# Kernel tuning notes

Measured on AMD Instinct MI355X. Metric: run time of the kernel, lower is better.

Reference implementation:

```python
import jax, jax.numpy as jnp
import numpy as np

SR = 16000
FRAME = 400      # int(0.025*SR)
HOP = 160        # int(0.01*SR)
MINP, MAXP = 32, 320   # SR/500, SR/50
NFFT_FRAME = 1024      # next pow2 >= 2*FRAME-1
NFFT_FULL = 262144     # >= samples + max hnr lag (160000+200)
LN_EPS = 1e-5


def _frame(a):
    n = a.shape[0]
    nf = (n - FRAME - 1) // HOP + 1  # len(range(0, n-FRAME, HOP))
    idx = jnp.arange(nf)[:, None] * HOP + jnp.arange(FRAME)[None, :]
    return a[idx]  # [nf, FRAME]


def _autocorr(x, nfft, nlags):
    # linear autocorrelation via FFT; nfft >= len + nlags avoids circular wrap
    X = jnp.fft.rfft(x, n=nfft)
    ac = jnp.fft.irfft(X * jnp.conj(X), n=nfft)
    return ac[..., :nlags]


def _masked_mean_std(x, m):
    cnt = m.sum()
    c = jnp.maximum(cnt, 1.0)
    mean = jnp.sum(x * m) / c
    var = jnp.sum(((x - mean) ** 2) * m) / c
    return jnp.where(cnt > 0, mean, 0.0), jnp.where(cnt > 0, jnp.sqrt(var), 0.0)


def _compact(vals, mask, fill_len):
    # pack masked values to the front (stable); first k=sum(mask) entries valid
    rank = jnp.cumsum(mask) - 1
    idx = jnp.where(mask, rank, fill_len)
    return jnp.zeros(fill_len, vals.dtype).at[idx].set(vals, mode='drop')


def _prosody_single(a):
    n = a.shape[0]
    frames = _frame(a)
    nf = frames.shape[0]
    # --- energy ---
    rms = jnp.sqrt(jnp.mean(frames ** 2, axis=-1))
    e_mean, e_std = rms.mean(), rms.std()
    # --- zero-crossing rate ---
    zcr = jnp.sum(jnp.abs(jnp.diff(jnp.sign(frames), axis=-1)), axis=-1) / (2.0 * FRAME)
    z_mean, z_std = zcr.mean(), zcr.std()
    # --- F0 via per-frame autocorrelation peak picking ---
    ac = _autocorr(frames, NFFT_FRAME, MAXP)            # [nf, 320]
    peak = jnp.argmax(ac[:, MINP:MAXP], axis=-1) + MINP  # first max, like np.argmax
    ac_pk = jnp.take_along_axis(ac, peak[:, None], axis=-1)[:, 0]
    f0 = SR / peak.astype(jnp.float32)
    valid = (ac_pk > 0.3 * ac[:, 0]) & (f0 > 50.0) & (f0 < 500.0)
    f0_mean, f0_std = _masked_mean_std(f0, valid.astype(jnp.float32))
    # --- jitter: rising threshold crossings over the whole waveform ---
    thr = 0.3 * jnp.max(jnp.abs(a))
    cross = (a[:-1] < thr) & (a[1:] >= thr)  # crossing at index i in [1, n)
    pos = jnp.arange(1, n)
    k = cross.sum()
    posarr = _compact(pos, cross, n)
    periods = (posarr[1:] - posarr[:-1]).astype(jnp.float32)
    nper = k - 1
    pmask = jnp.arange(n - 1) < nper
    mean_period = jnp.sum(periods * pmask) / jnp.maximum(nper, 1)
    pdiffs = jnp.abs(periods[1:] - periods[:-1])
    dmask = jnp.arange(n - 2) < (nper - 1)
    mean_pdiff = jnp.sum(pdiffs * dmask) / jnp.maximum(nper - 1, 1)
    jitter = jnp.where((nper >= 2) & (mean_period > 0),
                       jnp.clip(mean_pdiff / jnp.maximum(mean_period, 1e-12), 0.0, 1.0), 0.0)
    jitter = jnp.where((f0_mean < 50.0) | (f0_mean > 500.0), 0.0, jitter)
    # --- shimmer: diffs of consecutive retained (>0.01) frame peak amps ---
    amp = jnp.max(jnp.abs(frames), axis=-1)
    amask = amp > 0.01
    ka = amask.sum()
    amparr = _compact(amp, amask, nf)
    adiffs = jnp.abs(amparr[1:] - amparr[:-1])
    admask = jnp.arange(nf - 1) < (ka - 1)
    mean_amp = jnp.sum(amparr * (jnp.arange(nf) < ka)) / jnp.maximum(ka, 1)
    mean_adiff = jnp.sum(adiffs * admask) / jnp.maximum(ka - 1, 1)
    shimmer = jnp.where((ka >= 2) & (mean_amp > 0),
                        jnp.clip(mean_adiff / jnp.maximum(mean_amp, 1e-12), 0.0, 1.0), 0.0)
    # --- HNR: full-signal autocorrelation, lags 50..199 ---
    seg = _autocorr(a, NFFT_FULL, 200)[50:200]
    sig_peak = jnp.max(seg)
    noise_floor = jnp.percentile(seg, 10.0)  # numpy-default linear interpolation
    hnr = jnp.where(noise_floor > 0,
                    jnp.clip(sig_peak / jnp.maximum(noise_floor, 1e-30) / 100.0, 0.0, 1.0), 0.0)
    # --- voicing rate (energy + zcr thresholds; source truncated, see notes) ---
    voiced = (rms > 0.01) & (zcr < 0.3)
    voicing_rate = voiced.mean()
    feats = jnp.stack([f0_mean / 500.0, f0_std / 100.0, e_mean, e_std,
                       z_mean, z_std, jitter, shimmer, hnr, voicing_rate])
    metrics = jnp.stack([f0_mean, f0_std, e_mean, e_std, z_mean, z_std,
                         jitter, shimmer, hnr, voicing_rate])
    return feats, metrics


def _project(feats, W1, b1, gamma, beta, W2, b2):
    h = feats @ W1.T + b1
    mu = h.mean(-1, keepdims=True)
    var = h.var(-1, keepdims=True)
    h = (h - mu) / jnp.sqrt(var + LN_EPS) * gamma + beta
    h = jax.nn.relu(h)          # dropout = identity (eval mode)
    return h @ W2.T + b2


def setup_inputs() -> dict:
    key = jax.random.key(0)
    ks = jax.random.split(key, 7)
    B, N = 128, 160000
    return {
        'raw_audio': jax.random.normal(ks[0], (B, N), dtype=jnp.float32) * 0.5,
        'W1': jax.random.normal(ks[1], (64, 10), dtype=jnp.float32) * 0.3,
        'b1': jax.random.normal(ks[2], (64,), dtype=jnp.float32) * 0.01,
        'gamma': jnp.ones((64,), dtype=jnp.float32),
        'beta': jnp.zeros((64,), dtype=jnp.float32),
        'W2': jax.random.normal(ks[3], (128, 64), dtype=jnp.float32) * 0.1,
        'b2': jax.random.normal(ks[4], (128,), dtype=jnp.float32) * 0.01,
    }


def reference(raw_audio, W1, b1, gamma, beta, W2, b2):
    feats, metrics = jax.vmap(_prosody_single)(raw_audio)  # [B,10], [B,10]
    feats = jax.lax.stop_gradient(feats)  # torch detaches via numpy round-trip
    proj = _project(feats, W1, b1, gamma, beta, W2, b2)    # [B,128]
    return proj, metrics
```

## Files before the change

kernel.cpp:

```cpp
#include <hip/hip_runtime.h>
#include <stdint.h>

typedef unsigned int uint;
typedef unsigned short ushort;
typedef unsigned long long ull;
typedef __attribute__((ext_vector_type(8))) short bf16x8;
typedef __attribute__((ext_vector_type(4))) float f32x4;

#define SR_F 16000.0f
#define NSAMP 160000
#define NB 128
#define FRAME 400
#define HOP 160
#define NF 998
#define NHNR_CHUNK 10
#define JCH 125
#define HNR_LAGS 150
#define TJ 25
#define HWIN (32*TJ + 304)
#define NJB 10
#define TAIL0 ((NF - 1) * HOP + FRAME)

#define HXO 562
#define HREG 1116

#define OFF_RMS 0
#define OFF_ZCR (OFF_RMS + NB*NF)
#define OFF_AMP (OFF_ZCR + NB*NF)
#define OFF_F0  (OFF_AMP + NB*NF)
#define OFF_VAL (OFF_F0  + NB*NF)
#define OFF_HNR (OFF_VAL + NB*NF)
#define OFF_JST (OFF_HNR + NB*NHNR_CHUNK*HNR_LAGS)

__device__ __forceinline__ int imax_(int a, int b) { return a > b ? a : b; }
__device__ __forceinline__ int imin2_(int a, int b) { return a < b ? a : b; }

__device__ __forceinline__ int   f2i(float v) { return __builtin_bit_cast(int, v); }
__device__ __forceinline__ float i2f(int v)   { return __builtin_bit_cast(float, v); }
__device__ __forceinline__ uint  f2u(float v) { return __builtin_bit_cast(uint, v); }

#if __has_builtin(__builtin_amdgcn_permlane16_swap) && __has_builtin(__builtin_amdgcn_permlane32_swap)
#define HAVE_PLSWAP 1
#endif

template<int C>
__device__ __forceinline__ int dpp_i(int x) {
    return __builtin_amdgcn_update_dpp(0, x, C, 0xf, 0xf, true);
}
template<int C>
__device__ __forceinline__ float dpp_f(float x) { return i2f(dpp_i<C>(f2i(x))); }

__device__ __forceinline__ float wred_sum(float x) {
#ifdef HAVE_PLSWAP
    x += dpp_f<0xB1>(x);
    x += dpp_f<0x4E>(x);
    x += dpp_f<0x141>(x);
    x += dpp_f<0x140>(x);
    {
        auto r = __builtin_amdgcn_permlane16_swap(f2i(x), f2i(x), false, false);
        x = i2f((int)r[0]) + i2f((int)r[1]);
    }
    {
        auto r = __builtin_amdgcn_permlane32_swap(f2i(x), f2i(x), false, false);
        x = i2f((int)r[0]) + i2f((int)r[1]);
    }
#else
    #pragma unroll
    for (int off = 32; off; off >>= 1) x += __shfl_xor(x, off);
#endif
    return x;
}

__device__ __forceinline__ float wred_max(float x) {
#ifdef HAVE_PLSWAP
    x = fmaxf(x, dpp_f<0xB1>(x));
    x = fmaxf(x, dpp_f<0x4E>(x));
    x = fmaxf(x, dpp_f<0x141>(x));
    x = fmaxf(x, dpp_f<0x140>(x));
    {
        auto r = __builtin_amdgcn_permlane16_swap(f2i(x), f2i(x), false, false);
        x = fmaxf(i2f((int)r[0]), i2f((int)r[1]));
    }
    {
        auto r = __builtin_amdgcn_permlane32_swap(f2i(x), f2i(x), false, false);
        x = fmaxf(i2f((int)r[0]), i2f((int)r[1]));
    }
#else
    #pragma unroll
    for (int off = 32; off; off >>= 1) x = fmaxf(x, __shfl_xor(x, off));
#endif
    return x;
}

__device__ __forceinline__ int wred_imin(int x) {
#ifdef HAVE_PLSWAP
    x = imin2_(x, dpp_i<0xB1>(x));
    x = imin2_(x, dpp_i<0x4E>(x));
    x = imin2_(x, dpp_i<0x141>(x));
    x = imin2_(x, dpp_i<0x140>(x));
    {
        auto r = __builtin_amdgcn_permlane16_swap(x, x, false, false);
        x = imin2_((int)r[0], (int)r[1]);
    }
    {
        auto r = __builtin_amdgcn_permlane32_swap(x, x, false, false);
        x = imin2_((int)r[0], (int)r[1]);
    }
#else
    #pragma unroll
    for (int off = 32; off; off >>= 1) x = imin2_(x, __shfl_xor(x, off));
#endif
    return x;
}

__device__ __forceinline__ uint cvtpk_bf16(float a, float b) {
    uint r;
    asm("v_cvt_pk_bf16_f32 %0, %1, %2" : "=v"(r) : "v"(a), "v"(b));
    return r;
}

__device__ __forceinline__ bf16x8 ld_b_frag(const uint* p) {
    union { uint u[4]; bf16x8 v; } t;
    t.u[0] = p[0]; t.u[1] = p[1]; t.u[2] = p[2]; t.u[3] = p[3];
    return t.v;
}

__device__ __forceinline__ int sx_(float a, float b) {
    return (int)((f2u(a) ^ f2u(b)) >> 31);
}

struct JSt { int cnt, p0, p1, pl, pl2; float sum; };

__device__ __forceinline__ void jmerge(JSt& A, const JSt& r) {
    if (r.cnt == 0) return;
    if (A.cnt == 0) { A = r; return; }
    int pb = r.p0 - A.pl;
    A.sum += r.sum;
    if (A.cnt >= 2) A.sum += fabsf((float)(pb - (A.pl - A.pl2)));
    if (r.cnt >= 2) A.sum += fabsf((float)((r.p1 - r.p0) - pb));
    if (A.cnt == 1) A.p1 = r.p0;
    A.pl2 = (r.cnt >= 2) ? r.pl2 : A.pl;
    A.pl = r.pl;
    A.cnt += r.cnt;
}

__device__ __forceinline__ JSt jword(unsigned long long word, int wb) {
    JSt st; st.cnt = 0; st.p0 = 0; st.p1 = 0; st.pl = 0; st.pl2 = 0; st.sum = 0.f;
    while (word) {
        int b = __builtin_ctzll(word);
        word &= word - 1;
        int pos = wb + b + 1;
        if (st.cnt >= 2) st.sum += fabsf((float)((pos - st.pl) - (st.pl - st.pl2)));
        if (st.cnt == 0) st.p0 = pos;
        if (st.cnt == 1) st.p1 = pos;
        st.pl2 = st.pl; st.pl = pos; ++st.cnt;
    }
    return st;
}

__global__ __launch_bounds__(256) void k_frame(const float* __restrict__ audio,
                                               float* __restrict__ ws, int xoff)
{
    __shared__ __align__(16) uint lds[4][744];
    const int tid = threadIdx.x;
    const int widx = tid >> 6, lane = tid & 63;
    const int lo = lane & 15, q = lane >> 4;
    const int s = blockIdx.y;
    const int fbase = (blockIdx.x + xoff) * 16 + widx * 4;
    const float* as = audio + (size_t)s * NSAMP;

    uint* base = lds[widx];
    ull* zb = (ull*)base;
    const ushort* xw_us = (const ushort*)base;

    for (int i = lane; i < 168; i += 64) {
        int zi;
        if (i < 60)       zi = i;
        else if (i < 84)  zi = 160 + (i - 60);
        else if (i < 144) zi = 185 + (i - 84);
        else              zi = 345 + (i - 144);
        zb[zi] = 0ull;
    }

    float4 tA, tB; float bnA, bnB;
    {
        int f0 = fbase; if (f0 > NF - 1) f0 = NF - 1;
        const float* a = as + (size_t)f0 * HOP;
        tA  = ((const float4*)a)[lane];
        bnA = a[4 * lane + 4];
        tB.x = tB.y = tB.z = tB.w = 0.f; bnB = 0.f;
        if (lane < 36) {
            tB  = ((const float4*)a)[64 + lane];
            bnB = (lane < 35) ? a[4 * (64 + lane) + 4] : 0.f;
        }
    }

    for (int p = 0; p < 4; ++p) {
        int f = fbase + p; if (f > NF - 1) f = NF - 1;

        float amp; int zci;
        {
            amp = fmaxf(fmaxf(fabsf(tA.x), fabsf(tA.y)),
                        fmaxf(fabsf(tA.z), fabsf(tA.w)));
            zci = sx_(tA.x, tA.y) + sx_(tA.y, tA.z)
                + sx_(tA.z, tA.w) + sx_(tA.w, bnA);
            ull w = (ull)cvtpk_bf16(tA.x, tA.y) | ((ull)cvtpk_bf16(tA.z, tA.w) << 32);
            ull o = (ull)cvtpk_bf16(tA.y, tA.z) | ((ull)cvtpk_bf16(tA.w, bnA) << 32);
            zb[60 + lane]  = w;
            zb[245 + lane] = o;
        }
        if (lane < 36) {
            amp = fmaxf(amp, fmaxf(fmaxf(fabsf(tB.x), fabsf(tB.y)),
                                   fmaxf(fabsf(tB.z), fabsf(tB.w))));
            zci += sx_(tB.x, tB.y) + sx_(tB.y, tB.z) + sx_(tB.z, tB.w);
            if (lane < 35) zci += sx_(tB.w, bnB);
            ull w = (ull)cvtpk_bf16(tB.x, tB.y) | ((ull)cvtpk_bf16(tB.z, tB.w) << 32);
            ull o = (ull)cvtpk_bf16(tB.y, tB.z) | ((ull)cvtpk_bf16(tB.w, bnB) << 32);
            zb[124 + lane] = w;
            zb[309 + lane] = o;
        }
        float zcs = wred_sum((float)zci);
        amp = wred_max(amp);

        __syncthreads();

        float4 nA, nB; float nbA = 0.f, nbB = 0.f;
        nA.x = nA.y = nA.z = nA.w = 0.f; nB = nA;
        if (p < 3) {
            int fn = fbase + p + 1; if (fn > NF - 1) fn = NF - 1;
            const float* an = as + (size_t)fn * HOP;
            nA  = ((const float4*)an)[lane];
            nbA = an[4 * lane + 4];
            if (lane < 36) {
                nB  = ((const float4*)an)[64 + lane];
                nbB = (lane < 35) ? an[4 * (64 + lane) + 4] : 0.f;
            }
        }

        f32x4 acc1 = {0.f, 0.f, 0.f, 0.f};
        f32x4 acc2 = {0.f, 0.f, 0.f, 0.f};
        const int a_eb = 240 + 8 * q - 16 * lo;
        const uint* bp = base + ((lo & 1) ? 370 : 0) + 120 + 4 * q + (lo >> 1);
        bf16x8 ah[5];

        #pragma unroll
        for (int j = 0; j < 13; ++j) {
            bf16x8 a1 = *(const bf16x8*)(xw_us + a_eb + 32 * j);
            bf16x8 b  = ld_b_frag(bp + 16 * j);
            acc1 = __builtin_amdgcn_mfma_f32_16x16x32_bf16(a1, b, acc1, 0, 0, 0);
            if (j < 5) ah[j] = a1;
            if (j >= 8)
                acc2 = __builtin_amdgcn_mfma_f32_16x16x32_bf16(ah[j - 8], b, acc2, 0, 0, 0);
        }

        float ac0 = i2f(__builtin_amdgcn_readfirstlane(f2i(acc1[0])));

        float bv = -1e30f; int bl = 1 << 30;
        #pragma unroll
        for (int r = 0; r < 4; ++r) {
            int lag = 64 * q + 16 * r + lo;
            float v = acc1[r];
            bool ok = (r >= 2) || (q >= 1);
            if (ok && v > bv) { bv = v; bl = lag; }
        }
        if (q == 0) {
            #pragma unroll
            for (int r = 0; r < 4; ++r) {
                int lag = 256 + 16 * r + lo;
                float v = acc2[r];
                if (v > bv) { bv = v; bl = lag; }
            }
        }
        float mv = wred_max(bv);
        int   ml = wred_imin((bv == mv) ? bl : (1 << 30));

        if (lane == 0) {
            float f0v = SR_F / (float)ml;
            int valid = (mv > 0.3f * ac0) && (f0v > 50.f) && (f0v < 500.f);
            size_t idx = (size_t)s * NF + f;
            ws[OFF_RMS + idx] = sqrtf(fmaxf(ac0, 0.f) / (float)FRAME);
            ws[OFF_ZCR + idx] = zcs / 400.f;
            ws[OFF_AMP + idx] = amp;
            ws[OFF_F0  + idx] = f0v;
            ws[OFF_VAL + idx] = valid ? 1.f : 0.f;
        }

        tA = nA; tB = nB; bnA = nbA; bnB = nbB;
        __syncthreads();
    }
}

__global__ __launch_bounds__(256) void k_hnr(const float* __restrict__ audio,
                                             float* __restrict__ ws)
{
    __shared__ __align__(16) uint hxd[4][HREG];
    __shared__ unsigned long long msk[250];
    __shared__ __align__(16) uint pool[1504];
    __shared__ JSt sg[25];
    __shared__ float swmax[4];
    const int tid = threadIdx.x;
    const int widx = tid >> 6, lane = tid & 63;
    const int lo = lane & 15, q = lane >> 4;
    const int s = blockIdx.y;
    const int c = blockIdx.x * 4 + widx;
    const float* a = audio + (size_t)s * NSAMP;

    float (*hred)[152] = (float (*)[152])pool;
    JSt* sw = (JSt*)pool;

    uint* xwd = hxd[widx];
    uint* xod = hxd[widx] + HXO;
    const ushort* xw = (const ushort*)xwd;

    const int aoff = 240 + 8 * q - 16 * lo;
    const uint* bw = (lo & 1) ? xod : xwd;
    const int boff = 144 + 4 * q + (lo >> 1);

    f32x4 acc = {0.f, 0.f, 0.f, 0.f};

    for (int tile = 0; tile < JCH / TJ; ++tile) {
        const int g0 = 32 * (c * JCH + tile * TJ) - 288;
        for (int v = lane; v < HWIN / 4; v += 64) {
            int g = g0 + 4 * v;
            float x0, x1, x2, x3, x4;
            if (g >= 0 && g + 4 < NSAMP) {
                float4 t = *(const float4*)(a + g);
                x0 = t.x; x1 = t.y; x2 = t.z; x3 = t.w;
                x4 = a[g + 4];
            } else {
                x0 = (g     >= 0 && g     < NSAMP) ? a[g]     : 0.f;
                x1 = (g + 1 >= 0 && g + 1 < NSAMP) ? a[g + 1] : 0.f;
                x2 = (g + 2 >= 0 && g + 2 < NSAMP) ? a[g + 2] : 0.f;
                x3 = (g + 3 >= 0 && g + 3 < NSAMP) ? a[g + 3] : 0.f;
                x4 = (g + 4 >= 0 && g + 4 < NSAMP) ? a[g + 4] : 0.f;
            }
            int d = 2 * v;
            xwd[d] = cvtpk_bf16(x0, x1); xwd[d + 1] = cvtpk_bf16(x2, x3);
            xod[d] = cvtpk_bf16(x1, x2); xod[d + 1] = cvtpk_bf16(x3, x4);
        }
        asm volatile("" ::: "memory");
        __builtin_amdgcn_sched_barrier(0);

        #pragma unroll
        for (int jl = 0; jl < TJ; ++jl) {
            bf16x8 af = *(const bf16x8*)(xw + aoff + 32 * jl);
            bf16x8 bf = ld_b_frag(bw + boff + 16 * jl);
            acc = __builtin_amdgcn_mfma_f32_16x16x32_bf16(af, bf, acc, 0, 0, 0);
        }
        asm volatile("" ::: "memory");
        __builtin_amdgcn_sched_barrier(0);
    }

    #pragma unroll
    for (int r = 0; r < 4; ++r) {
        int row = 4 * q + r;
        int lag = 48 + 16 * row + lo;
        if (row < 10 && lag >= 50 && lag < 200)
            hred[widx][lag - 50] = acc[r];
    }
    __syncthreads();
    if (tid < HNR_LAGS) {
        float v = hred[0][tid] + hred[1][tid] + hred[2][tid] + hred[3][tid];
        ws[OFF_HNR + ((size_t)s * NHNR_CHUNK + blockIdx.x) * HNR_LAGS + tid] = v;
    }

    float m = 0.f;
    const float* ampA = ws + OFF_AMP + (size_t)s * NF;
    for (int i = tid; i < NF; i += 256) m = fmaxf(m, ampA[i]);
    if (tid < NSAMP - TAIL0) m = fmaxf(m, fabsf(a[TAIL0 + tid]));
    m = wred_max(m);
    if ((tid & 63) == 0) swmax[tid >> 6] = m;
    __syncthreads();
    const float thr = 0.3f * fmaxf(fmaxf(swmax[0], swmax[1]),
                                   fmaxf(swmax[2], swmax[3]));

    const int cbase = blockIdx.x * 16000;
    for (int ot = 0; ot < 9; ++ot) {
        float va[7], vb[7];
        #pragma unroll
        for (int k = 0; k < 7; ++k) {
            int off = (ot * 7 + k) * 256 + tid;
            int i = cbase + off;
            bool in = (off < 16000) && (i < NSAMP - 1);
            va[k] = in ? a[i] : 1e30f;
            vb[k] = in ? a[i + 1] : 1e30f;
        }
        #pragma unroll
        for (int k = 0; k < 7; ++k) {
            int off = (ot * 7 + k) * 256 + tid;
            bool fl = (va[k] < thr) && (vb[k] >= thr);
            unsigned long long bal = __ballot(fl);
            int w = off >> 6;
            if ((tid & 63) == 0 && w < 250) msk[w] = bal;
        }
    }
    __syncthreads();

    if (tid < 250) sw[tid] = jword(msk[tid], cbase + tid * 64);
    __syncthreads();
    if (tid < 25) {
        JSt A = sw[10 * tid];
        #pragma unroll
        for (int k = 1; k < 10; ++k) jmerge(A, sw[10 * tid + k]);
        sg[tid] = A;
    }
    __syncthreads();
    if (tid == 0) {
        JSt A = sg[0];
        for (int k = 1; k < 25; ++k) jmerge(A, sg[k]);
        float* jp = ws + OFF_JST + ((size_t)s * NJB + blockIdx.x) * 6;
        jp[0] = (float)A.cnt; jp[1] = (float)A.p0; jp[2] = (float)A.p1;
        jp[3] = (float)A.pl;  jp[4] = (float)A.pl2; jp[5] = A.sum;
    }
}

__global__ __launch_bounds__(256) void k_final(const float* __restrict__ ws,
        const float* __restrict__ W1, const float* __restrict__ b1,
        const float* __restrict__ gam, const float* __restrict__ bet,
        const float* __restrict__ W2, const float* __restrict__ b2,
        float* __restrict__ out)
{
    __shared__ float samp[NF];
    __shared__ float sac[HNR_LAGS];
    __shared__ float sred[32];
    __shared__ float sstat[11];
    __shared__ float sjit[4];
    __shared__ float sjst[NJB * 6];
    __shared__ float sfeats[10];
    __shared__ float shid[64];
    __shared__ float ssa[250][5];
    __shared__ float ssg[25][5];

    const int s = blockIdx.x;
    const int tid = threadIdx.x;
    const float* rmsA = ws + OFF_RMS + (size_t)s * NF;
    const float* zcrA = ws + OFF_ZCR + (size_t)s * NF;
    const float* ampA = ws + OFF_AMP + (size_t)s * NF;
    const float* f0A  = ws + OFF_F0  + (size_t)s * NF;
    const float* valA = ws + OFF_VAL + (size_t)s * NF;

    float a0=0,a1=0,a2=0,a3=0,a4=0,a5=0,a6=0,a7=0;
    for (int i = tid; i < NF; i += 256) {
        float r = rmsA[i], z = zcrA[i], f0 = f0A[i], v = valA[i];
        samp[i] = ampA[i];
        a0 += r; a1 += r * r; a2 += z; a3 += z * z;
        a4 += f0 * v; a5 += f0 * f0 * v; a6 += v;
        a7 += (r > 0.01f && z < 0.3f) ? 1.f : 0.f;
    }
    if (tid < NJB * 6) sjst[tid] = ws[OFF_JST + (size_t)s * NJB * 6 + tid];
    #pragma unroll
    for (int off = 32; off; off >>= 1) {
        a0 += __shfl_xor(a0, off); a1 += __shfl_xor(a1, off);
        a2 += __shfl_xor(a2, off); a3 += __shfl_xor(a3, off);
        a4 += __shfl_xor(a4, off); a5 += __shfl_xor(a5, off);
        a6 += __shfl_xor(a6, off); a7 += __shfl_xor(a7, off);
    }
    if ((tid & 63) == 0) {
        int w = tid >> 6;
        sred[w*8+0]=a0; sred[w*8+1]=a1; sred[w*8+2]=a2; sred[w*8+3]=a3;
        sred[w*8+4]=a4; sred[w*8+5]=a5; sred[w*8+6]=a6; sred[w*8+7]=a7;
    }
    __syncthreads();

    if (tid < HNR_LAGS) {
        float acc = 0.f;
        const float* p = ws + OFF_HNR + (size_t)s * NHNR_CHUNK * HNR_LAGS + tid;
        #pragma unroll
        for (int c = 0; c < NHNR_CHUNK; ++c) acc += p[c * HNR_LAGS];
        sac[tid] = acc;
    }
    if (tid == 0) {
        for (int k = 0; k < 8; ++k)
            sstat[k] = sred[k] + sred[8+k] + sred[16+k] + sred[24+k];
    }
    if (tid < 250) {
        int i0 = tid * 4;
        float cnt=0.f, first=0.f, last=0.f, ssum=0.f, sad=0.f;
        #pragma unroll
        for (int k = 0; k < 4; ++k) {
            int i = i0 + k;
            if (i < NF) {
                float av = samp[i];
                if (av > 0.01f) {
                    if (cnt >= 1.f) sad += fabsf(av - last);
                    else first = av;
                    ssum += av; last = av; cnt += 1.f;
                }
            }
        }
        ssa[tid][0]=cnt; ssa[tid][1]=first; ssa[tid][2]=last;
        ssa[tid][3]=ssum; ssa[tid][4]=sad;
    }
    __syncthreads();

    if (tid < HNR_LAGS) {
        float v = sac[tid];
        int r = 0;
        for (int j = 0; j < HNR_LAGS; ++j) {
            float vj = sac[j];
            r += (vj < v) || (vj == v && j < tid);
        }
        if (r == 14) sstat[8] = v;
        if (r == 15) sstat[9] = v;
    }
    if (tid == 160) {
        JSt A; A.cnt = 0; A.p0 = 0; A.p1 = 0; A.pl = 0; A.pl2 = 0; A.sum = 0.f;
        for (int c = 0; c < NJB; ++c) {
            JSt r;
            r.cnt = (int)sjst[c*6+0]; r.p0 = (int)sjst[c*6+1];
            r.p1  = (int)sjst[c*6+2]; r.pl = (int)sjst[c*6+3];
            r.pl2 = (int)sjst[c*6+4]; r.sum = sjst[c*6+5];
            jmerge(A, r);
        }
        sjit[0] = (float)A.cnt; sjit[1] = (float)A.p0;
        sjit[2] = (float)A.pl;  sjit[3] = A.sum;
    }
    if (tid == 192) {
        float mx = sac[0];
        for (int j = 1; j < HNR_LAGS; ++j) mx = fmaxf(mx, sac[j]);
        sstat[10] = mx;
    }
    if (tid >= 200 && tid < 225) {
        int t2 = tid - 200;
        float cnt=0.f, first=0.f, last=0.f, ssum=0.f, sad=0.f;
        #pragma unroll
        for (int k = 0; k < 10; ++k) {
            int j = 10 * t2 + k;
            float c2 = ssa[j][0];
            if (c2 > 0.f) {
                if (cnt > 0.f) sad += ssa[j][4] + fabsf(ssa[j][1] - last);
                else { first = ssa[j][1]; sad += ssa[j][4]; }
                ssum += ssa[j][3]; last = ssa[j][2]; cnt += c2;
            }
        }
        ssg[t2][0]=cnt; ssg[t2][1]=first; ssg[t2][2]=last;
        ssg[t2][3]=ssum; ssg[t2][4]=sad;
    }
    __syncthreads();

    if (tid == 0) {
        float S_r = sstat[0], S_r2 = sstat[1], S_z = sstat[2], S_z2 = sstat[3];
        float S_f = sstat[4], S_f2 = sstat[5], S_v = sstat[6], S_voi = sstat[7];
        float e_mean = S_r / (float)NF;
        float e_std  = sqrtf(fmaxf(S_r2 / (float)NF - e_mean * e_mean, 0.f));
        float z_mean = S_z / (float)NF;
        float z_std  = sqrtf(fmaxf(S_z2 / (float)NF - z_mean * z_mean, 0.f));
        float f0_mean = 0.f, f0_std = 0.f;
        if (S_v > 0.f) {
            f0_mean = S_f / S_v;
            f0_std  = sqrtf(fmaxf(S_f2 / S_v - f0_mean * f0_mean, 0.f));
        }
        int k = (int)sjit[0];
        float pp0 = sjit[1], ppl = sjit[2], psum = sjit[3];
        int nper = k - 1;
        float mean_period = (k >= 2) ? (ppl - pp0) / (float)(k - 1) : 0.f;
        float mean_pd = psum / (float)imax_(nper - 1, 1);
        float jit = (nper >= 2 && mean_period > 0.f)
            ? fminf(fmaxf(mean_pd / fmaxf(mean_period, 1e-12f), 0.f), 1.f) : 0.f;
        if (f0_mean < 50.f || f0_mean > 500.f) jit = 0.f;
        float noise = 0.1f * sstat[8] + 0.9f * sstat[9];
        float hnr = (noise > 0.f)
            ? fminf(fmaxf(sstat[10] / fmaxf(noise, 1e-30f) / 100.f, 0.f), 1.f) : 0.f;

        float cnt=0.f, first=0.f, last=0.f, ssum=0.f, sad=0.f;
        for (int c = 0; c < 25; ++c) {
            float c2 = ssg[c][0];
            if (c2 > 0.f) {
                if (cnt > 0.f) sad += ssg[c][4] + fabsf(ssg[c][1] - last);
                else { first = ssg[c][1]; sad += ssg[c][4]; }
                ssum += ssg[c][3]; last = ssg[c][2]; cnt += c2;
            }
        }
        int ka = (int)cnt;
        float mean_amp = ssum / (float)imax_(ka, 1);
        float mean_ad  = sad  / (float)imax_(ka - 1, 1);
        float shim = (ka >= 2 && mean_amp > 0.f)
            ? fminf(fmaxf(mean_ad / fmaxf(mean_amp, 1e-12f), 0.f), 1.f) : 0.f;
        float voice = S_voi / (float)NF;

        float mt[10] = {f0_mean, f0_std, e_mean, e_std, z_mean, z_std, jit, shim, hnr, voice};
        for (int i = 0; i < 10; ++i) out[NB * 128 + s * 10 + i] = mt[i];
        sfeats[0] = f0_mean / 500.f;
        sfeats[1] = f0_std / 100.f;
        for (int i = 2; i < 10; ++i) sfeats[i] = mt[i];
    }
    __syncthreads();

    if (tid < 64) {
        float h = b1[tid];
        #pragma unroll
        for (int i = 0; i < 10; ++i) h = fmaf(sfeats[i], W1[tid * 10 + i], h);
        float sum = h, sq = h * h;
        #pragma unroll
        for (int off = 32; off; off >>= 1) {
            sum += __shfl_xor(sum, off);
            sq  += __shfl_xor(sq, off);
        }
        float mu = sum / 64.f;
        float var = sq / 64.f - mu * mu;
        float hn = (h - mu) * rsqrtf(var + 1e-5f) * gam[tid] + bet[tid];
        shid[tid] = fmaxf(hn, 0.f);
    }
    __syncthreads();
    if (tid < 128) {
        float accv = b2[tid];
        #pragma unroll 8
        for (int j = 0; j < 64; ++j) accv = fmaf(shid[j], W2[tid * 64 + j], accv);
        out[(size_t)s * 128 + tid] = accv;
    }
}

extern "C" void kernel_launch(void* const* d_in, const int* in_sizes, int n_in,
                              void* d_out, int out_size, void* d_ws, size_t ws_size,
                              hipStream_t stream)
{
    const float* audio = (const float*)d_in[0];
    const float* W1    = (const float*)d_in[1];
    const float* b1    = (const float*)d_in[2];
    const float* gam   = (const float*)d_in[3];
    const float* bet   = (const float*)d_in[4];
    const float* W2    = (const float*)d_in[5];
    const float* b2    = (const float*)d_in[6];
    float* out = (float*)d_out;
    float* ws  = (float*)d_ws;

    hipLaunchKernelGGL(k_frame, dim3(32, NB), dim3(256), 0, stream, audio, ws, 0);
    hipLaunchKernelGGL(k_frame, dim3(31, NB), dim3(256), 0, stream, audio, ws, 32);
    hipLaunchKernelGGL(k_hnr,   dim3(NJB, NB), dim3(256), 0, stream, audio, ws);
    hipLaunchKernelGGL(k_final, dim3(NB),      dim3(256), 0, stream,
                       ws, W1, b1, gam, bet, W2, b2, out);
}
```

Baseline: 241.7 us.

## Merge frame and HNR autocorrelation work into one launch, split jitter out

The two per-frame launches and the HNR autocorrelation are now issued as a single grid. The first 63 blocks per sample do frame features and the remaining 10 do HNR lag sums. The jitter threshold-crossing pass, which needs the per-frame amplitude maxima, moves into its own kernel after that launch. The aim is to cut launch count and serial gaps and let HNR blocks overlap frame blocks. It adds one extra launch for jitter, and the shared LDS union may lower occupancy for the frame blocks.

Result: faster. 231.3 us (-4.3%).

```diff
diff --git a/kernel.cpp b/kernel.cpp
--- a/kernel.cpp
+++ b/kernel.cpp
@@ -19,6 +19,7 @@
 #define TJ 25
 #define HWIN (32*TJ + 304)
 #define NJB 10
+#define NFB 63
 #define TAIL0 ((NF - 1) * HOP + FRAME)
 
 #define HXO 562
@@ -158,211 +159,208 @@
     return st;
 }
 
-__global__ __launch_bounds__(256) void k_frame(const float* __restrict__ audio,
-                                               float* __restrict__ ws, int xoff)
+__global__ __launch_bounds__(256) void k_main(const float* __restrict__ audio,
+                                              float* __restrict__ ws)
 {
-    __shared__ __align__(16) uint lds[4][744];
+    __shared__ __align__(16) uint shm[5072];
     const int tid = threadIdx.x;
     const int widx = tid >> 6, lane = tid & 63;
     const int lo = lane & 15, q = lane >> 4;
     const int s = blockIdx.y;
-    const int fbase = (blockIdx.x + xoff) * 16 + widx * 4;
     const float* as = audio + (size_t)s * NSAMP;
 
-    uint* base = lds[widx];
-    ull* zb = (ull*)base;
-    const ushort* xw_us = (const ushort*)base;
-
-    for (int i = lane; i < 168; i += 64) {
-        int zi;
-        if (i < 60)       zi = i;
-        else if (i < 84)  zi = 160 + (i - 60);
-        else if (i < 144) zi = 185 + (i - 84);
-        else              zi = 345 + (i - 144);
-        zb[zi] = 0ull;
-    }
-
-    float4 tA, tB; float bnA, bnB;
-    {
-        int f0 = fbase; if (f0 > NF - 1) f0 = NF - 1;
-        const float* a = as + (size_t)f0 * HOP;
-        tA  = ((const float4*)a)[lane];
-        bnA = a[4 * lane + 4];
-        tB.x = tB.y = tB.z = tB.w = 0.f; bnB = 0.f;
-        if (lane < 36) {
-            tB  = ((const float4*)a)[64 + lane];
-            bnB = (lane < 35) ? a[4 * (64 + lane) + 4] : 0.f;
-        }
-    }
-
-    for (int p = 0; p < 4; ++p) {
-        int f = fbase + p; if (f > NF - 1) f = NF - 1;
-
-        float amp; int zci;
+    if (blockIdx.x < NFB) {
+        uint* base = shm + widx * 744;
+        ull* zb = (ull*)base;
+        const ushort* xw_us = (const ushort*)base;
+        const int fbase = blockIdx.x * 16 + widx * 4;
+
+        for (int i = lane; i < 168; i += 64) {
+            int zi;
+            if (i < 60)       zi = i;
+            else if (i < 84)  zi = 160 + (i - 60);
+            else if (i < 144) zi = 185 + (i - 84);
+            else              zi = 345 + (i - 144);
+            zb[zi] = 0ull;
+        }
+
+        float4 tA, tB; float bnA, bnB;
         {
-            amp = fmaxf(fmaxf(fabsf(tA.x), fabsf(tA.y)),
-                        fmaxf(fabsf(tA.z), fabsf(tA.w)));
-            zci = sx_(tA.x, tA.y) + sx_(tA.y, tA.z)
-                + sx_(tA.z, tA.w) + sx_(tA.w, bnA);
-            ull w = (ull)cvtpk_bf16(tA.x, tA.y) | ((ull)cvtpk_bf16(tA.z, tA.w) << 32);
-            ull o = (ull)cvtpk_bf16(tA.y, tA.z) | ((ull)cvtpk_bf16(tA.w, bnA) << 32);
-            zb[60 + lane]  = w;
-            zb[245 + lane] = o;
-        }
-        if (lane < 36) {
-            amp = fmaxf(amp, fmaxf(fmaxf(fabsf(tB.x), fabsf(tB.y)),
-                                   fmaxf(fabsf(tB.z), fabsf(tB.w))));
-            zci += sx_(tB.x, tB.y) + sx_(tB.y, tB.z) + sx_(tB.z, tB.w);
-            if (lane < 35) zci += sx_(tB.w, bnB);
-            ull w = (ull)cvtpk_bf16(tB.x, tB.y) | ((ull)cvtpk_bf16(tB.z, tB.w) << 32);
-            ull o = (ull)cvtpk_bf16(tB.y, tB.z) | ((ull)cvtpk_bf16(tB.w, bnB) << 32);
-            zb[124 + lane] = w;
-            zb[309 + lane] = o;
-        }
-        float zcs = wred_sum((float)zci);
-        amp = wred_max(amp);
-
-        __syncthreads();
-
-        float4 nA, nB; float nbA = 0.f, nbB = 0.f;
-        nA.x = nA.y = nA.z = nA.w = 0.f; nB = nA;
-        if (p < 3) {
-            int fn = fbase + p + 1; if (fn > NF - 1) fn = NF - 1;
-            const float* an = as + (size_t)fn * HOP;
-            nA  = ((const float4*)an)[lane];
-            nbA = an[4 * lane + 4];
+            int f0 = fbase; if (f0 > NF - 1) f0 = NF - 1;
+            const float* a = as + (size_t)f0 * HOP;
+            tA  = ((const float4*)a)[lane];
+            bnA = a[4 * lane + 4];
+            tB.x = tB.y = tB.z = tB.w = 0.f; bnB = 0.f;
             if (lane < 36) {
-                nB  = ((const float4*)an)[64 + lane];
-                nbB = (lane < 35) ? an[4 * (64 + lane) + 4] : 0.f;
-            }
-        }
-
-        f32x4 acc1 = {0.f, 0.f, 0.f, 0.f};
-        f32x4 acc2 = {0.f, 0.f, 0.f, 0.f};
-        const int a_eb = 240 + 8 * q - 16 * lo;
-        const uint* bp = base + ((lo & 1) ? 370 : 0) + 120 + 4 * q + (lo >> 1);
-        bf16x8 ah[5];
-
-        #pragma unroll
-        for (int j = 0; j < 13; ++j) {
-            bf16x8 a1 = *(const bf16x8*)(xw_us + a_eb + 32 * j);
-            bf16x8 b  = ld_b_frag(bp + 16 * j);
-            acc1 = __builtin_amdgcn_mfma_f32_16x16x32_bf16(a1, b, acc1, 0, 0, 0);
-            if (j < 5) ah[j] = a1;
-            if (j >= 8)
-                acc2 = __builtin_amdgcn_mfma_f32_16x16x32_bf16(ah[j - 8], b, acc2, 0, 0, 0);
-        }
-
-        float ac0 = i2f(__builtin_amdgcn_readfirstlane(f2i(acc1[0])));
-
-        float bv = -1e30f; int bl = 1 << 30;
-        #pragma unroll
-        for (int r = 0; r < 4; ++r) {
-            int lag = 64 * q + 16 * r + lo;
-            float v = acc1[r];
-            bool ok = (r >= 2) || (q >= 1);
-            if (ok && v > bv) { bv = v; bl = lag; }
-        }
-        if (q == 0) {
+                tB  = ((const float4*)a)[64 + lane];
+                bnB = (lane < 35) ? a[4 * (64 + lane) + 4] : 0.f;
+            }
+        }
+
+        for (int p = 0; p < 4; ++p) {
+            int f = fbase + p; if (f > NF - 1) f = NF - 1;
+
+            float amp; int zci;
+            {
+                amp = fmaxf(fmaxf(fabsf(tA.x), fabsf(tA.y)),
+                            fmaxf(fabsf(tA.z), fabsf(tA.w)));
+                zci = sx_(tA.x, tA.y) + sx_(tA.y, tA.z)
+                    + sx_(tA.z, tA.w) + sx_(tA.w, bnA);
+                ull w = (ull)cvtpk_bf16(tA.x, tA.y) | ((ull)cvtpk_bf16(tA.z, tA.w) << 32);
+                ull o = (ull)cvtpk_bf16(tA.y, tA.z) | ((ull)cvtpk_bf16(tA.w, bnA) << 32);
+                zb[60 + lane]  = w;
+                zb[245 + lane] = o;
+            }
+            if (lane < 36) {
+                amp = fmaxf(amp, fmaxf(fmaxf(fabsf(tB.x), fabsf(tB.y)),
+                                       fmaxf(fabsf(tB.z), fabsf(tB.w))));
+                zci += sx_(tB.x, tB.y) + sx_(tB.y, tB.z) + sx_(tB.z, tB.w);
+                if (lane < 35) zci += sx_(tB.w, bnB);
+                ull w = (ull)cvtpk_bf16(tB.x, tB.y) | ((ull)cvtpk_bf16(tB.z, tB.w) << 32);
+                ull o = (ull)cvtpk_bf16(tB.y, tB.z) | ((ull)cvtpk_bf16(tB.w, bnB) << 32);
+                zb[124 + lane] = w;
+                zb[309 + lane] = o;
+            }
+            float zcs = wred_sum((float)zci);
+            amp = wred_max(amp);
+
+            __syncthreads();
+
+            float4 nA, nB; float nbA = 0.f, nbB = 0.f;
+            nA.x = nA.y = nA.z = nA.w = 0.f; nB = nA;
+            if (p < 3) {
+                int fn = fbase + p + 1; if (fn > NF - 1) fn = NF - 1;
+                const float* an = as + (size_t)fn * HOP;
+                nA  = ((const float4*)an)[lane];
+                nbA = an[4 * lane + 4];
+                if (lane < 36) {
+                    nB  = ((const float4*)an)[64 + lane];
+                    nbB = (lane < 35) ? an[4 * (64 + lane) + 4] : 0.f;
+                }
+            }
+
+            f32x4 acc1 = {0.f, 0.f, 0.f, 0.f};
+            f32x4 acc2 = {0.f, 0.f, 0.f, 0.f};
+            const int a_eb = 240 + 8 * q - 16 * lo;
+            const uint* bp = base + ((lo & 1) ? 370 : 0) + 120 + 4 * q + (lo >> 1);
+            bf16x8 ah[5];
+
+            #pragma unroll
+            for (int j = 0; j < 13; ++j) {
+                bf16x8 a1 = *(const bf16x8*)(xw_us + a_eb + 32 * j);
+                bf16x8 b  = ld_b_frag(bp + 16 * j);
+                acc1 = __builtin_amdgcn_mfma_f32_16x16x32_bf16(a1, b, acc1, 0, 0, 0);
+                if (j < 5) ah[j] = a1;
+                if (j >= 8)
+                    acc2 = __builtin_amdgcn_mfma_f32_16x16x32_bf16(ah[j - 8], b, acc2, 0, 0, 0);
+            }
+
+            float ac0 = i2f(__builtin_amdgcn_readfirstlane(f2i(acc1[0])));
+
+            float bv = -1e30f; int bl = 1 << 30;
             #pragma unroll
             for (int r = 0; r < 4; ++r) {
-                int lag = 256 + 16 * r + lo;
-                float v = acc2[r];
-                if (v > bv) { bv = v; bl = lag; }
-            }
-        }
-        float mv = wred_max(bv);
-        int   ml = wred_imin((bv == mv) ? bl : (1 << 30));
-
-        if (lane == 0) {
-            float f0v = SR_F / (float)ml;
-            int valid = (mv > 0.3f * ac0) && (f0v > 50.f) && (f0v < 500.f);
-            size_t idx = (size_t)s * NF + f;
-            ws[OFF_RMS + idx] = sqrtf(fmaxf(ac0, 0.f) / (float)FRAME);
-            ws[OFF_ZCR + idx] = zcs / 400.f;
-            ws[OFF_AMP + idx] = amp;
-            ws[OFF_F0  + idx] = f0v;
-            ws[OFF_VAL + idx] = valid ? 1.f : 0.f;
-        }
-
-        tA = nA; tB = nB; bnA = nbA; bnB = nbB;
+                int lag = 64 * q + 16 * r + lo;
+                float v = acc1[r];
+                bool ok = (r >= 2) || (q >= 1);
+                if (ok && v > bv) { bv = v; bl = lag; }
+            }
+            if (q == 0) {
+                #pragma unroll
+                for (int r = 0; r < 4; ++r) {
+                    int lag = 256 + 16 * r + lo;
+                    float v = acc2[r];
+                    if (v > bv) { bv = v; bl = lag; }
+                }
+            }
+            float mv = wred_max(bv);
+            int   ml = wred_imin((bv == mv) ? bl : (1 << 30));
+
+            if (lane == 0) {
+                float f0v = SR_F / (float)ml;
+                int valid = (mv > 0.3f * ac0) && (f0v > 50.f) && (f0v < 500.f);
+                size_t idx = (size_t)s * NF + f;
+                ws[OFF_RMS + idx] = sqrtf(fmaxf(ac0, 0.f) / (float)FRAME);
+                ws[OFF_ZCR + idx] = zcs / 400.f;
+                ws[OFF_AMP + idx] = amp;
+                ws[OFF_F0  + idx] = f0v;
+                ws[OFF_VAL + idx] = valid ? 1.f : 0.f;
+            }
+
+            tA = nA; tB = nB; bnA = nbA; bnB = nbB;
+            __syncthreads();
+        }
+    } else {
+        const int bxh = blockIdx.x - NFB;
+        const int c = bxh * 4 + widx;
+        uint* xwd = shm + widx * HREG;
+        uint* xod = xwd + HXO;
+        const ushort* xw = (const ushort*)xwd;
+        float (*hred)[152] = (float (*)[152])(shm + 4464);
+
+        const int aoff = 240 + 8 * q - 16 * lo;
+        const uint* bw = (lo & 1) ? xod : xwd;
+        const int boff = 144 + 4 * q + (lo >> 1);
+
+        f32x4 acc = {0.f, 0.f, 0.f, 0.f};
+
+        for (int tile = 0; tile < JCH / TJ; ++tile) {
+            const int g0 = 32 * (c * JCH + tile * TJ) - 288;
+            for (int v = lane; v < HWIN / 4; v += 64) {
+                int g = g0 + 4 * v;
+                float x0, x1, x2, x3, x4;
+                if (g >= 0 && g + 4 < NSAMP) {
+                    float4 t = *(const float4*)(as + g);
+                    x0 = t.x; x1 = t.y; x2 = t.z; x3 = t.w;
+                    x4 = as[g + 4];
+                } else {
+                    x0 = (g     >= 0 && g     < NSAMP) ? as[g]     : 0.f;
+                    x1 = (g + 1 >= 0 && g + 1 < NSAMP) ? as[g + 1] : 0.f;
+                    x2 = (g + 2 >= 0 && g + 2 < NSAMP) ? as[g + 2] : 0.f;
+                    x3 = (g + 3 >= 0 && g + 3 < NSAMP) ? as[g + 3] : 0.f;
+                    x4 = (g + 4 >= 0 && g + 4 < NSAMP) ? as[g + 4] : 0.f;
+                }
+                int d = 2 * v;
+                xwd[d] = cvtpk_bf16(x0, x1); xwd[d + 1] = cvtpk_bf16(x2, x3);
+                xod[d] = cvtpk_bf16(x1, x2); xod[d + 1] = cvtpk_bf16(x3, x4);
+            }
+            asm volatile("" ::: "memory");
+            __builtin_amdgcn_sched_barrier(0);
+
+            #pragma unroll
+            for (int jl = 0; jl < TJ; ++jl) {
+                bf16x8 af = *(const bf16x8*)(xw + aoff + 32 * jl);
+                bf16x8 bf = ld_b_frag(bw + boff + 16 * jl);
+                acc = __builtin_amdgcn_mfma_f32_16x16x32_bf16(af, bf, acc, 0, 0, 0);
+            }
+            asm volatile("" ::: "memory");
+            __builtin_amdgcn_sched_barrier(0);
+        }
+
+        #pragma unroll
+        for (int r = 0; r < 4; ++r) {
+            int row = 4 * q + r;
+            int lag = 48 + 16 * row + lo;
+            if (row < 10 && lag >= 50 && lag < 200)
+                hred[widx][lag - 50] = acc[r];
+        }
         __syncthreads();
-    }
-}
-
-__global__ __launch_bounds__(256) void k_hnr(const float* __restrict__ audio,
+        if (tid < HNR_LAGS) {
+            float v = hred[0][tid] + hred[1][tid] + hred[2][tid] + hred[3][tid];
+            ws[OFF_HNR + ((size_t)s * NHNR_CHUNK + bxh) * HNR_LAGS + tid] = v;
+        }
+    }
+}
+
+__global__ __launch_bounds__(256) void k_jit(const float* __restrict__ audio,
                                              float* __restrict__ ws)
 {
-    __shared__ __align__(16) uint hxd[4][HREG];
     __shared__ unsigned long long msk[250];
-    __shared__ __align__(16) uint pool[1504];
+    __shared__ JSt sw[250];
     __shared__ JSt sg[25];
     __shared__ float swmax[4];
-    const int tid = threadIdx.x;
-    const int widx = tid >> 6, lane = tid & 63;
-    const int lo = lane & 15, q = lane >> 4;
-    const int s = blockIdx.y;
-    const int c = blockIdx.x * 4 + widx;
+    const int s = blockIdx.y, b = blockIdx.x, tid = threadIdx.x;
     const float* a = audio + (size_t)s * NSAMP;
-
-    float (*hred)[152] = (float (*)[152])pool;
-    JSt* sw = (JSt*)pool;
-
-    uint* xwd = hxd[widx];
-    uint* xod = hxd[widx] + HXO;
-    const ushort* xw = (const ushort*)xwd;
-
-    const int aoff = 240 + 8 * q - 16 * lo;
-    const uint* bw = (lo & 1) ? xod : xwd;
-    const int boff = 144 + 4 * q + (lo >> 1);
-
-    f32x4 acc = {0.f, 0.f, 0.f, 0.f};
-
-    for (int tile = 0; tile < JCH / TJ; ++tile) {
-        const int g0 = 32 * (c * JCH + tile * TJ) - 288;
-        for (int v = lane; v < HWIN / 4; v += 64) {
-            int g = g0 + 4 * v;
-            float x0, x1, x2, x3, x4;
-            if (g >= 0 && g + 4 < NSAMP) {
-                float4 t = *(const float4*)(a + g);
-                x0 = t.x; x1 = t.y; x2 = t.z; x3 = t.w;
-                x4 = a[g + 4];
-            } else {
-                x0 = (g     >= 0 && g     < NSAMP) ? a[g]     : 0.f;
-                x1 = (g + 1 >= 0 && g + 1 < NSAMP) ? a[g + 1] : 0.f;
-                x2 = (g + 2 >= 0 && g + 2 < NSAMP) ? a[g + 2] : 0.f;
-                x3 = (g + 3 >= 0 && g + 3 < NSAMP) ? a[g + 3] : 0.f;
-                x4 = (g + 4 >= 0 && g + 4 < NSAMP) ? a[g + 4] : 0.f;
-            }
-            int d = 2 * v;
-            xwd[d] = cvtpk_bf16(x0, x1); xwd[d + 1] = cvtpk_bf16(x2, x3);
-            xod[d] = cvtpk_bf16(x1, x2); xod[d + 1] = cvtpk_bf16(x3, x4);
-        }
-        asm volatile("" ::: "memory");
-        __builtin_amdgcn_sched_barrier(0);
-
-        #pragma unroll
-        for (int jl = 0; jl < TJ; ++jl) {
-            bf16x8 af = *(const bf16x8*)(xw + aoff + 32 * jl);
-            bf16x8 bf = ld_b_frag(bw + boff + 16 * jl);
-            acc = __builtin_amdgcn_mfma_f32_16x16x32_bf16(af, bf, acc, 0, 0, 0);
-        }
-        asm volatile("" ::: "memory");
-        __builtin_amdgcn_sched_barrier(0);
-    }
-
-    #pragma unroll
-    for (int r = 0; r < 4; ++r) {
-        int row = 4 * q + r;
-        int lag = 48 + 16 * row + lo;
-        if (row < 10 && lag >= 50 && lag < 200)
-            hred[widx][lag - 50] = acc[r];
-    }
-    __syncthreads();
-    if (tid < HNR_LAGS) {
-        float v = hred[0][tid] + hred[1][tid] + hred[2][tid] + hred[3][tid];
-        ws[OFF_HNR + ((size_t)s * NHNR_CHUNK + blockIdx.x) * HNR_LAGS + tid] = v;
-    }
 
     float m = 0.f;
     const float* ampA = ws + OFF_AMP + (size_t)s * NF;
@@ -374,7 +372,7 @@
     const float thr = 0.3f * fmaxf(fmaxf(swmax[0], swmax[1]),
                                    fmaxf(swmax[2], swmax[3]));
 
-    const int cbase = blockIdx.x * 16000;
+    const int cbase = b * 16000;
     for (int ot = 0; ot < 9; ++ot) {
         float va[7], vb[7];
         #pragma unroll
@@ -408,7 +406,7 @@
     if (tid == 0) {
         JSt A = sg[0];
         for (int k = 1; k < 25; ++k) jmerge(A, sg[k]);
-        float* jp = ws + OFF_JST + ((size_t)s * NJB + blockIdx.x) * 6;
+        float* jp = ws + OFF_JST + ((size_t)s * NJB + b) * 6;
         jp[0] = (float)A.cnt; jp[1] = (float)A.p0; jp[2] = (float)A.p1;
         jp[3] = (float)A.pl;  jp[4] = (float)A.pl2; jp[5] = A.sum;
     }
@@ -624,9 +622,8 @@
     float* out = (float*)d_out;
     float* ws  = (float*)d_ws;
 
-    hipLaunchKernelGGL(k_frame, dim3(32, NB), dim3(256), 0, stream, audio, ws, 0);
-    hipLaunchKernelGGL(k_frame, dim3(31, NB), dim3(256), 0, stream, audio, ws, 32);
-    hipLaunchKernelGGL(k_hnr,   dim3(NJB, NB), dim3(256), 0, stream, audio, ws);
-    hipLaunchKernelGGL(k_final, dim3(NB),      dim3(256), 0, stream,
+    hipLaunchKernelGGL(k_main,  dim3(NFB + NJB, NB), dim3(256), 0, stream, audio, ws);
+    hipLaunchKernelGGL(k_jit,   dim3(NJB, NB),       dim3(256), 0, stream, audio, ws);
+    hipLaunchKernelGGL(k_final, dim3(NB),            dim3(256), 0, stream,
                        ws, W1, b1, gam, bet, W2, b2, out);
 }
```
